# Kernel tuning notes

Hardware: AMD Instinct MI355X
Metric: run time of the kernel (lower is better)

## Reference

```python
import jax, jax.numpy as jnp
import numpy as np

B, S, D, H, T = 64, 512, 768, 384, 22  # batch, seq, bert dim, lstm hidden, tagset+2


def setup_inputs() -> dict:
    key = jax.random.key(0)
    ks = jax.random.split(key, 14)
    hidden_states = jax.random.normal(ks[0], (B, S, D), jnp.float32)
    # strictly increasing wordpiece start offsets, -1 padded (per-sample variable length)
    nw = np.array([S // 2 - (b % 16) * 4 for b in range(B)])  # number of valid start ids
    sid = -np.ones((B, S), np.int64)
    msk = np.zeros((B, S), np.int64)
    for b in range(B):
        sid[b, : nw[b]] = 1 + 2 * np.arange(nw[b])  # max = 2*nw-1 <= S-1
        msk[b, : nw[b] + 1] = 1  # word-level mask: nw+1 words incl. CLS slot
    start_ids = jnp.asarray(sid)
    masks = jnp.asarray(msk)
    sc = 0.05
    h0 = jax.random.normal(ks[1], (2, B, H), jnp.float32)
    c0 = jax.random.normal(ks[2], (2, B, H), jnp.float32)
    W_ih_f = jax.random.normal(ks[3], (4 * H, D), jnp.float32) * sc
    W_hh_f = jax.random.normal(ks[4], (4 * H, H), jnp.float32) * sc
    b_ih_f = jax.random.normal(ks[5], (4 * H,), jnp.float32) * sc
    b_hh_f = jax.random.normal(ks[6], (4 * H,), jnp.float32) * sc
    W_ih_b = jax.random.normal(ks[7], (4 * H, D), jnp.float32) * sc
    W_hh_b = jax.random.normal(ks[8], (4 * H, H), jnp.float32) * sc
    b_ih_b = jax.random.normal(ks[9], (4 * H,), jnp.float32) * sc
    b_hh_b = jax.random.normal(ks[10], (4 * H,), jnp.float32) * sc
    W_lin = jax.random.normal(ks[11], (T, 2 * H), jnp.float32) * sc
    b_lin = jax.random.normal(ks[12], (T,), jnp.float32) * sc
    return {"hidden_states": hidden_states, "h0": h0, "c0": c0,
            "W_ih_f": W_ih_f, "W_hh_f": W_hh_f, "b_ih_f": b_ih_f, "b_hh_f": b_hh_f,
            "W_ih_b": W_ih_b, "W_hh_b": W_hh_b, "b_ih_b": b_ih_b, "b_hh_b": b_hh_b,
            "W_lin": W_lin, "b_lin": b_lin, "start_ids": start_ids, "masks": masks}


def _lstm_dir(x, h0, c0, Wih, Whh, bih, bhh, reverse):
    # x: [B,S,D]; torch gate order i,f,g,o
    xg = jnp.einsum('bsd,gd->bsg', x, Wih) + bih + bhh  # [B,S,4H]
    xs = jnp.swapaxes(xg, 0, 1)  # [S,B,4H]
    if reverse:
        xs = xs[::-1]

    def step(carry, xt):
        h, c = carry
        g = xt + h @ Whh.T
        i, f, gg, o = jnp.split(g, 4, axis=-1)
        c = jax.nn.sigmoid(f) * c + jax.nn.sigmoid(i) * jnp.tanh(gg)
        h = jax.nn.sigmoid(o) * jnp.tanh(c)
        return (h, c), h

    _, hs = jax.lax.scan(step, (h0, c0), xs)
    if reverse:
        hs = hs[::-1]
    return jnp.swapaxes(hs, 0, 1)  # [B,S,H]


def _align(hidden_states, start_ids, masks):
    # word t embedding: t==0 -> token 0 (CLS); 1<=t<n -> token start_ids[t]-1
    # (last wordpiece of word t); t==n -> token start_ids[n-1]; else zero-pad.
    Bb, Ss, _ = hidden_states.shape
    t = jnp.arange(Ss)[None, :]
    valid = start_ids >= 0
    n = valid.sum(-1)  # [B] number of valid start ids
    last_sid = jnp.take_along_axis(start_ids, (n - 1)[:, None], axis=1)  # [B,1]
    idx = jnp.where(t == 0, 0,
          jnp.where(t < n[:, None], start_ids - 1,
          jnp.where(t == n[:, None], last_sid, 0)))
    idx = jnp.clip(idx, 0, Ss - 1)
    gathered = jnp.take_along_axis(hidden_states, idx[:, :, None], axis=1)
    sent_len = masks.sum(-1)  # word-level lengths (second loop in torch code)
    keep = (t < sent_len[:, None])[:, :, None]
    return jnp.where(keep, gathered, 0.0)


def reference(hidden_states, h0, c0, W_ih_f, W_hh_f, b_ih_f, b_hh_f,
              W_ih_b, W_hh_b, b_ih_b, b_hh_b, W_lin, b_lin, start_ids, masks):
    embeds = _align(hidden_states, start_ids, masks)  # q=1,k=0 => wordpiece-only
    hf = _lstm_dir(embeds, h0[0], c0[0], W_ih_f, W_hh_f, b_ih_f, b_hh_f, False)
    hb = _lstm_dir(embeds, h0[1], c0[1], W_ih_b, W_hh_b, b_ih_b, b_hh_b, True)
    lstm_out = jnp.concatenate([hf, hb], axis=-1)  # [B,S,2H]
    # dropout1 is identity in eval mode
    feats = lstm_out @ W_lin.T + b_lin  # [B,S,T]
    return feats
```

## Files before the change

### kernel.cpp

```cpp
#include <hip/hip_runtime.h>

typedef unsigned short u16;
typedef unsigned int u32;
typedef unsigned long long u64;

typedef short bf16x8 __attribute__((ext_vector_type(8)));
typedef float f32x4 __attribute__((ext_vector_type(4)));
typedef u32 u32x4 __attribute__((ext_vector_type(4)));

#define NB 64
#define NS 512
#define ND 768
#define NH 384
#define NT_OUT 22
#define S2 272
#define NG 1536
#define MGEMM (NB*S2)
#define MAGIC 0x5A5AA5A5u
#define MAX_RETRY 1000000
#define NQC 6

__device__ __forceinline__ u16 f2b(float f) {
    u32 u = __float_as_uint(f);
    u32 r = (u + 0x7fffu + ((u >> 16) & 1u)) >> 16;
    return (u16)r;
}
__device__ __forceinline__ float b2f(u16 s) { return __uint_as_float(((u32)s) << 16); }

__device__ __forceinline__ float sigm(float x) {
    return __builtin_amdgcn_rcpf(1.f + __expf(-x));
}
__device__ __forceinline__ float tanh_(float x) {
    return 1.f - 2.f * __builtin_amdgcn_rcpf(1.f + __expf(2.f * x));
}

__device__ __forceinline__ void gl_lds16(const void* g, void* l) {
    __builtin_amdgcn_global_load_lds(
        (const __attribute__((address_space(1))) unsigned int*)g,
        (__attribute__((address_space(3))) unsigned int*)l, 16, 0, 0);
}

__device__ __forceinline__ u32 ld_sc0(const int* p) {
    u32 v;
    asm volatile("global_load_dword %0, %1, off sc0 nt\n\t"
                 "s_waitcnt vmcnt(0)"
                 : "=&v"(v) : "v"(p) : "memory");
    return v;
}
__device__ __forceinline__ void st_sc0(int* p, u32 v) {
    asm volatile("global_store_dword %0, %1, off sc0" :: "v"(p), "v"(v) : "memory");
}

__device__ __forceinline__ void ld4_fast_nw(const u32* p,
        u32x4& A, u32x4& B, u32x4& C, u32x4& D) {
    asm volatile(
        "global_load_dwordx4 %0, %4, off sc0 nt\n\t"
        "global_load_dwordx4 %1, %4, off offset:16 sc0 nt\n\t"
        "global_load_dwordx4 %2, %4, off offset:128 sc0 nt\n\t"
        "global_load_dwordx4 %3, %4, off offset:144 sc0 nt"
        : "=&v"(A), "=&v"(B), "=&v"(C), "=&v"(D)
        : "v"(p) : "memory");
}
__device__ __forceinline__ void ld4_fast_wt(const u32* p,
        u32x4& A, u32x4& B, u32x4& C, u32x4& D) {
    asm volatile(
        "global_load_dwordx4 %0, %4, off sc0 nt\n\t"
        "global_load_dwordx4 %1, %4, off offset:16 sc0 nt\n\t"
        "global_load_dwordx4 %2, %4, off offset:128 sc0 nt\n\t"
        "global_load_dwordx4 %3, %4, off offset:144 sc0 nt\n\t"
        "s_waitcnt vmcnt(0)"
        : "=&v"(A), "=&v"(B), "=&v"(C), "=&v"(D)
        : "v"(p) : "memory");
}
__device__ __forceinline__ void ld4_slow(const u32* p,
        u32x4& A, u32x4& B, u32x4& C, u32x4& D) {
    #pragma unroll
    for (int e = 0; e < 4; e++) {
        A[e] = __hip_atomic_load(p + e,      __ATOMIC_RELAXED, __HIP_MEMORY_SCOPE_AGENT);
        B[e] = __hip_atomic_load(p + 4 + e,  __ATOMIC_RELAXED, __HIP_MEMORY_SCOPE_AGENT);
        C[e] = __hip_atomic_load(p + 32 + e, __ATOMIC_RELAXED, __HIP_MEMORY_SCOPE_AGENT);
        D[e] = __hip_atomic_load(p + 36 + e, __ATOMIC_RELAXED, __HIP_MEMORY_SCOPE_AGENT);
    }
}
__device__ __forceinline__ void ld4_nw(bool fast, const u32* p,
        u32x4& A, u32x4& B, u32x4& C, u32x4& D) {
    if (fast) ld4_fast_nw(p, A, B, C, D);
    else      ld4_slow(p, A, B, C, D);
}
__device__ __forceinline__ void ld4_wt(bool fast, const u32* p,
        u32x4& A, u32x4& B, u32x4& C, u32x4& D) {
    if (fast) ld4_fast_wt(p, A, B, C, D);
    else      ld4_slow(p, A, B, C, D);
}
__device__ __forceinline__ void st4(bool fast, u32* p, u32x4 v) {
    if (fast)
        asm volatile("global_store_dwordx4 %0, %1, off sc0" :: "v"(p), "v"(v) : "memory");
    else {
        #pragma unroll
        for (int e = 0; e < 4; e++)
            __hip_atomic_store(p + e, v[e], __ATOMIC_RELAXED, __HIP_MEMORY_SCOPE_AGENT);
    }
}
#define WAIT_VM(N) do { __builtin_amdgcn_sched_barrier(0); \
    asm volatile("s_waitcnt vmcnt(" #N ")" ::: "memory"); \
    __builtin_amdgcn_sched_barrier(0); } while (0)
__device__ __forceinline__ void ldsbar() {
    asm volatile("s_waitcnt lgkmcnt(0)" ::: "memory");
    __builtin_amdgcn_s_barrier();
    __builtin_amdgcn_sched_barrier(0);
}

__device__ __forceinline__ u32 sum4(const u32x4& a, const u32x4& b,
                                    const u32x4& c, const u32x4& d) {
    u32 s = (a[0] & 0xffffu) + (a[1] & 0xffffu) + (a[2] & 0xffffu) + (a[3] & 0xffffu);
    s += (b[0] & 0xffffu) + (b[1] & 0xffffu) + (b[2] & 0xffffu) + (b[3] & 0xffffu);
    s += (c[0] & 0xffffu) + (c[1] & 0xffffu) + (c[2] & 0xffffu) + (c[3] & 0xffffu);
    s += (d[0] & 0xffffu) + (d[1] & 0xffffu) + (d[2] & 0xffffu) + (d[3] & 0xffffu);
    return s;
}
__device__ __forceinline__ bf16x8 packf(const u32x4& lo, const u32x4& hi) {
    union { u32 q[4]; bf16x8 v; } U;
    U.q[0] = __builtin_amdgcn_perm(lo[1], lo[0], 0x07060302u);
    U.q[1] = __builtin_amdgcn_perm(lo[3], lo[2], 0x07060302u);
    U.q[2] = __builtin_amdgcn_perm(hi[1], hi[0], 0x07060302u);
    U.q[3] = __builtin_amdgcn_perm(hi[3], hi[2], 0x07060302u);
    return U.v;
}

__global__ void k_prep(const float* __restrict__ hidden, const int* __restrict__ start_ids,
                       const int* __restrict__ masks, u16* __restrict__ embeds) {
    int b = blockIdx.x >> 2;
    int quarter = blockIdx.x & 3;
    int tid = threadIdx.x;
    __shared__ int red[256];
    int cn = 0, cm = 0;
    for (int s = tid; s < NS; s += 256) {
        cn += (start_ids[b * NS + s] >= 0) ? 1 : 0;
        cm += (masks[b * NS + s] != 0) ? 1 : 0;
    }
    red[tid] = cn + (cm << 16);
    __syncthreads();
    #pragma unroll
    for (int off = 128; off > 0; off >>= 1) {
        if (tid < off) red[tid] += red[tid + off];
        __syncthreads();
    }
    int n = red[0] & 0xffff;
    int slen = red[0] >> 16;
    n = min(max(n, 1), NS);
    int last = start_ids[b * NS + n - 1];
    for (int t = quarter * 68; t < quarter * 68 + 68; ++t) {
        int idx;
        if (t == 0) idx = 0;
        else if (t < n) idx = start_ids[b * NS + t] - 1;
        else if (t == n) idx = last;
        else idx = 0;
        idx = min(max(idx, 0), NS - 1);
        bool keep = t < slen;
        const float* src = hidden + ((size_t)b * NS + idx) * ND;
        u16* dst = embeds + ((size_t)b * S2 + t) * ND;
        if (tid < 192) {
            float4 v = keep ? *(const float4*)(src + tid * 4) : make_float4(0.f, 0.f, 0.f, 0.f);
            union { u16 u[4]; uint2 q; } pk;
            pk.u[0] = f2b(v.x); pk.u[1] = f2b(v.y); pk.u[2] = f2b(v.z); pk.u[3] = f2b(v.w);
            *(uint2*)(dst + tid * 4) = pk.q;
        }
    }
}

__global__ void k_weights(const float* __restrict__ wf, const float* __restrict__ wb,
                          const float* __restrict__ bihf, const float* __restrict__ bhhf,
                          const float* __restrict__ bihb, const float* __restrict__ bhhb,
                          const float* __restrict__ h0,
                          u16* __restrict__ wihcat, float* __restrict__ biascat,
                          u16* __restrict__ h0buf) {
    int i0 = blockIdx.x * blockDim.x + threadIdx.x;
    int NTH = gridDim.x * blockDim.x;
    for (size_t i = i0; i < (size_t)2 * NG * ND; i += NTH) {
        size_t nrow = i / ND, k = i - nrow * ND;
        float v = (nrow < NG) ? wf[nrow * ND + k] : wb[(nrow - NG) * ND + k];
        wihcat[i] = f2b(v);
    }
    for (int i = i0; i < 2 * NG; i += NTH)
        biascat[i] = (i < NG) ? bihf[i] + bhhf[i] : bihb[i - NG] + bhhb[i - NG];
    for (int i = i0; i < 2 * NB * NH; i += NTH) h0buf[i] = f2b(h0[i]);
}

__global__ void k_packwhh(const float* __restrict__ whhf, const float* __restrict__ whhb,
                          u16* __restrict__ pack) {
    int ft = blockIdx.x * 256 + threadIdx.x;
    if (ft >= 2 * NQC * 4 * 4 * 12 * 64) return;
    int lane = ft & 63;
    int grp = ft >> 6;
    int ks = grp % 12; grp /= 12;
    int nt = grp & 3;  grp >>= 2;
    int w  = grp & 3;  grp >>= 2;
    int qc = grp % NQC;
    int d  = grp / NQC;
    const float* W = d ? whhb : whhf;
    int col = w * NH + qc * 64 + nt * 16 + (lane & 15);
    int k0 = ks * 32 + (lane >> 4) * 8;
    u16* dst = pack + (size_t)ft * 8;
    #pragma unroll
    for (int e = 0; e < 8; e++) dst[e] = f2b(W[(size_t)col * NH + k0 + e]);
}

__launch_bounds__(256, 2)
__global__ void k_gemm(const u16* __restrict__ A, const u16* __restrict__ Bw,
                       const float* __restrict__ biascat, u16* __restrict__ xg) {
    __shared__ u16 As[128 * 32];
    __shared__ u16 Bs[128 * 32];
    int tid = threadIdx.x;
    int lane = tid & 63, wid = tid >> 6;
    int l15 = lane & 15, q4 = lane >> 4;
    int bn = blockIdx.x;
    int bm = blockIdx.y;
    int wm = (wid >> 1) * 64, wn = (wid & 1) * 64;
    f32x4 acc[4][4] = {};
    for (int k0 = 0; k0 < ND; k0 += 32) {
        #pragma unroll
        for (int j = 0; j < 2; j++) {
            int fl = tid + j * 256;
            int row = fl >> 2, cb = fl & 3;
            const u16* ga = A + (size_t)(bm * 128 + row) * ND + k0 + cb * 8;
            gl_lds16(ga, &As[(size_t)(wid * 64 + j * 256) * 8]);
            const u16* gb = Bw + (size_t)(bn * 128 + row) * ND + k0 + cb * 8;
            gl_lds16(gb, &Bs[(size_t)(wid * 64 + j * 256) * 8]);
        }
        __syncthreads();
        bf16x8 af[4], bf[4];
        #pragma unroll
        for (int mt = 0; mt < 4; mt++)
            af[mt] = *(const bf16x8*)&As[(wm + mt * 16 + l15) * 32 + q4 * 8];
        #pragma unroll
        for (int nt = 0; nt < 4; nt++)
            bf[nt] = *(const bf16x8*)&Bs[(wn + nt * 16 + l15) * 32 + q4 * 8];
        #pragma unroll
        for (int mt = 0; mt < 4; mt++)
            #pragma unroll
            for (int nt = 0; nt < 4; nt++)
                acc[mt][nt] = __builtin_amdgcn_mfma_f32_16x16x32_bf16(af[mt], bf[nt], acc[mt][nt], 0, 0, 0);
        __syncthreads();
    }
    #pragma unroll
    for (int nt = 0; nt < 4; nt++) {
        int gn = bn * 128 + wn + nt * 16 + l15;
        int d = gn >= NG ? 1 : 0;
        int col = gn - d * NG;
        float bias = biascat[gn];
        #pragma unroll
        for (int mt = 0; mt < 4; mt++) {
            #pragma unroll
            for (int r = 0; r < 4; r++) {
                int m = bm * 128 + wm + mt * 16 + q4 * 4 + r;
                int b = m / S2, t = m - b * S2;
                float v = acc[mt][nt][r] + bias;
                xg[((size_t)(d * NB + b) * S2 + t) * NG + col] = f2b(v);
            }
        }
    }
}

__launch_bounds__(256, 1)
__global__ void k_recur(const u16* __restrict__ whhpack, const u16* __restrict__ xg,
                        const float* __restrict__ biascat, const u16* __restrict__ h0buf,
                        const float* __restrict__ c0, u16* __restrict__ hout,
                        int* __restrict__ flags, u32* __restrict__ xch) {
    const int blk = blockIdx.x;
    const int qc = blk >> 3;
    const int cl = blk & 7;
    const int d = cl >> 2;
    const int g = cl & 3;
    const int tid = threadIdx.x, lane = tid & 63, w = tid >> 6;
    const int q4 = lane >> 4, l15 = lane & 15;

    __shared__ float preact[4 * 16 * 68];
    __shared__ u16 hlds[16 * 72];
    __shared__ int s_fast;

    bf16x8 bfr[4][12];
    #pragma unroll
    for (int nt = 0; nt < 4; nt++)
        #pragma unroll
        for (int j = 0; j < 12; j++) {
            int ksg = 2 * ((qc + (j >> 1)) % NQC) + (j & 1);
            bfr[nt][j] = *(const bf16x8*)(whhpack +
                ((size_t)((((d * NQC + qc) * 4 + w) * 4 + nt) * 12 + ksg) * 64 + lane) * 8);
        }

    const int bb = tid >> 4;
    const int jo = (tid & 15) * 4;
    float cre[4];
    {
        const float* cp = c0 + (size_t)(d * NB + g * 16 + bb) * NH + qc * 64 + jo;
        #pragma unroll
        for (int e = 0; e < 4; e++) cre[e] = cp[e];
    }
    float biasreg[4];
    #pragma unroll
    for (int nt = 0; nt < 4; nt++)
        biasreg[nt] = biascat[d * NG + w * NH + qc * 64 + nt * 16 + l15];

    if (tid == 0) {
        int* pzb = flags + cl * 128;
        int* pmb = flags + 2048 + cl * 128;
        st_sc0(pzb + qc * 16, MAGIC);
        u32 seen = 1u << qc;
        for (int spin = 0; spin < 768 && seen != 0x3Fu; ++spin) {
            #pragma unroll
            for (int r = 0; r < NQC; ++r)
                if (!((seen >> r) & 1u) && ld_sc0(pzb + r * 16) == MAGIC) seen |= 1u << r;
            __builtin_amdgcn_s_sleep(2);
        }
        __hip_atomic_store(pmb + qc * 16, (int)(0x100u | seen),
                           __ATOMIC_RELAXED, __HIP_MEMORY_SCOPE_AGENT);
        u32 m = 0x3Fu;
        int spin2 = 0;
        #pragma unroll
        for (int r = 0; r < NQC; ++r) {
            u32 v;
            do {
                v = (u32)__hip_atomic_load(pmb + r * 16, __ATOMIC_RELAXED,
                                           __HIP_MEMORY_SCOPE_AGENT);
            } while (!(v & 0x100u) && ++spin2 < MAX_RETRY);
            m &= v;
        }
        s_fast = ((m & 0x3Fu) == 0x3Fu && spin2 < MAX_RETRY) ? 1 : 0;
    }
    __syncthreads();
    const bool fast = (s_fast != 0);

    const u16* xgd = xg + (size_t)d * NB * S2 * NG;

    float ci[4][4];
    auto preload = [&](int it2) {
        int s2 = d ? (NS - 1 - it2) : it2;
        if (s2 < S2) {
            const u16* xrow = xgd + ((size_t)(g * 16) * S2 + s2) * NG + w * NH + qc * 64 + l15;
            #pragma unroll
            for (int nt = 0; nt < 4; nt++)
                #pragma unroll
                for (int r = 0; r < 4; r++)
                    ci[nt][r] = b2f(xrow[(size_t)(q4 * 4 + r) * S2 * NG + nt * 16]);
        } else {
            #pragma unroll
            for (int nt = 0; nt < 4; nt++)
                #pragma unroll
                for (int r = 0; r < 4; r++) ci[nt][r] = biasreg[nt];
        }
    };
    preload(0);

    #pragma unroll 1
    for (int it = 0; it < NS; ++it) {
        int s = d ? (NS - 1 - it) : it;
        f32x4 acc[4];

        if (it == 0) {
            bf16x8 af0[12];
            const u16* hp = h0buf + (size_t)(d * NB + g * 16) * NH;
            #pragma unroll
            for (int j = 0; j < 12; j++) {
                int ksg = 2 * ((qc + (j >> 1)) % NQC) + (j & 1);
                af0[j] = *(const bf16x8*)(hp + (size_t)l15 * NH + ksg * 32 + q4 * 8);
            }
            #pragma unroll
            for (int nt = 0; nt < 4; nt++) {
                acc[nt][0] = ci[nt][0]; acc[nt][1] = ci[nt][1];
                acc[nt][2] = ci[nt][2]; acc[nt][3] = ci[nt][3];
            }
            preload(1);
            #pragma unroll
            for (int j = 0; j < 12; j++)
                #pragma unroll
                for (int nt = 0; nt < 4; nt++)
                    acc[nt] = __builtin_amdgcn_mfma_f32_16x16x32_bf16(af0[j], bfr[nt][j], acc[nt], 0, 0, 0);
        } else {
            const u32 T = (u32)it;
            const u32 want = T * 16u;
            u32* xb = xch + (size_t)((T & 3u) * 8 + cl) * (NQC * 1024)
                          + (u32)(l15 * 64 + q4 * 8);
            u32* p1 = xb + ((qc + 1) % NQC) * 1024;
            u32* p2 = xb + ((qc + 2) % NQC) * 1024;
            u32* p3 = xb + ((qc + 3) % NQC) * 1024;
            u32* p4 = xb + ((qc + 4) % NQC) * 1024;
            u32* p5 = xb + ((qc + 5) % NQC) * 1024;
            u32x4 r10, r11, r12, r13, r20, r21, r22, r23, r30, r31, r32, r33;
            u32x4 r40, r41, r42, r43, r50, r51, r52, r53;
            ld4_nw(fast, p1, r10, r11, r12, r13);
            ld4_nw(fast, p2, r20, r21, r22, r23);
            ld4_nw(fast, p3, r30, r31, r32, r33);
            ld4_nw(fast, p4, r40, r41, r42, r43);
            ld4_nw(fast, p5, r50, r51, r52, r53);
            bf16x8 afo0 = *(const bf16x8*)&hlds[l15 * 72 + q4 * 8];
            bf16x8 afo1 = *(const bf16x8*)&hlds[l15 * 72 + 32 + q4 * 8];
            #pragma unroll
            for (int nt = 0; nt < 4; nt++) {
                acc[nt][0] = ci[nt][0]; acc[nt][1] = ci[nt][1];
                acc[nt][2] = ci[nt][2]; acc[nt][3] = ci[nt][3];
            }
            #pragma unroll
            for (int nt = 0; nt < 4; nt++)
                acc[nt] = __builtin_amdgcn_mfma_f32_16x16x32_bf16(afo0, bfr[nt][0], acc[nt], 0, 0, 0);
            #pragma unroll
            for (int nt = 0; nt < 4; nt++)
                acc[nt] = __builtin_amdgcn_mfma_f32_16x16x32_bf16(afo1, bfr[nt][1], acc[nt], 0, 0, 0);
            int tries;
            WAIT_VM(16);
            tries = 0;
            while (!__all(sum4(r10, r11, r12, r13) == want) && ++tries < MAX_RETRY)
                ld4_wt(fast, p1, r10, r11, r12, r13);
            {
                bf16x8 lo = packf(r10, r11), hi = packf(r12, r13);
                #pragma unroll
                for (int nt = 0; nt < 4; nt++)
                    acc[nt] = __builtin_amdgcn_mfma_f32_16x16x32_bf16(lo, bfr[nt][2], acc[nt], 0, 0, 0);
                #pragma unroll
                for (int nt = 0; nt < 4; nt++)
                    acc[nt] = __builtin_amdgcn_mfma_f32_16x16x32_bf16(hi, bfr[nt][3], acc[nt], 0, 0, 0);
            }
            WAIT_VM(12);
            tries = 0;
            while (!__all(sum4(r20, r21, r22, r23) == want) && ++tries < MAX_RETRY)
                ld4_wt(fast, p2, r20, r21, r22, r23);
            {
                bf16x8 lo = packf(r20, r21), hi = packf(r22, r23);
                #pragma unroll
                for (int nt = 0; nt < 4; nt++)
                    acc[nt] = __builtin_amdgcn_mfma_f32_16x16x32_bf16(lo, bfr[nt][4], acc[nt], 0, 0, 0);
                #pragma unroll
                for (int nt = 0; nt < 4; nt++)
                    acc[nt] = __builtin_amdgcn_mfma_f32_16x16x32_bf16(hi, bfr[nt][5], acc[nt], 0, 0, 0);
            }
            WAIT_VM(8);
            tries = 0;
            while (!__all(sum4(r30, r31, r32, r33) == want) && ++tries < MAX_RETRY)
                ld4_wt(fast, p3, r30, r31, r32, r33);
            {
                bf16x8 lo = packf(r30, r31), hi = packf(r32, r33);
                #pragma unroll
                for (int nt = 0; nt < 4; nt++)
                    acc[nt] = __builtin_amdgcn_mfma_f32_16x16x32_bf16(lo, bfr[nt][6], acc[nt], 0, 0, 0);
                #pragma unroll
                for (int nt = 0; nt < 4; nt++)
                    acc[nt] = __builtin_amdgcn_mfma_f32_16x16x32_bf16(hi, bfr[nt][7], acc[nt], 0, 0, 0);
            }
            WAIT_VM(4);
            tries = 0;
            while (!__all(sum4(r40, r41, r42, r43) == want) && ++tries < MAX_RETRY)
                ld4_wt(fast, p4, r40, r41, r42, r43);
            {
                bf16x8 lo = packf(r40, r41), hi = packf(r42, r43);
                #pragma unroll
                for (int nt = 0; nt < 4; nt++)
                    acc[nt] = __builtin_amdgcn_mfma_f32_16x16x32_bf16(lo, bfr[nt][8], acc[nt], 0, 0, 0);
                #pragma unroll
                for (int nt = 0; nt < 4; nt++)
                    acc[nt] = __builtin_amdgcn_mfma_f32_16x16x32_bf16(hi, bfr[nt][9], acc[nt], 0, 0, 0);
            }
            WAIT_VM(0);
            tries = 0;
            while (!__all(sum4(r50, r51, r52, r53) == want) && ++tries < MAX_RETRY)
                ld4_wt(fast, p5, r50, r51, r52, r53);
            if (it + 1 < NS) preload(it + 1);
            {
                bf16x8 lo = packf(r50, r51), hi = packf(r52, r53);
                #pragma unroll
                for (int nt = 0; nt < 4; nt++)
                    acc[nt] = __builtin_amdgcn_mfma_f32_16x16x32_bf16(lo, bfr[nt][10], acc[nt], 0, 0, 0);
                #pragma unroll
                for (int nt = 0; nt < 4; nt++)
                    acc[nt] = __builtin_amdgcn_mfma_f32_16x16x32_bf16(hi, bfr[nt][11], acc[nt], 0, 0, 0);
            }
        }

        #pragma unroll
        for (int nt = 0; nt < 4; nt++)
            #pragma unroll
            for (int r = 0; r < 4; r++)
                preact[w * 1088 + (q4 * 4 + r) * 68 + nt * 16 + l15] = acc[nt][r];
        ldsbar();

        {
            int ib = bb * 68 + jo;
            u16* ho = hout + (((size_t)(d * NB + g * 16 + bb)) * NS + s) * NH + qc * 64 + jo;
            union { u16 u[4]; uint2 q; } pk;
            u32x4 tg;
            u32 t2 = (u32)it + 1u;
            #pragma unroll
            for (int e = 0; e < 4; e++) {
                float gi = preact[0 * 1088 + ib + e], gf = preact[1 * 1088 + ib + e];
                float gg = preact[2 * 1088 + ib + e], go = preact[3 * 1088 + ib + e];
                float c = cre[e];
                float cn = sigm(gf) * c + sigm(gi) * tanh_(gg);
                float hn = sigm(go) * tanh_(cn);
                cre[e] = cn;
                pk.u[e] = f2b(hn);
                tg[e] = ((u32)pk.u[e] << 16) | t2;
            }
            u32* xp = xch + (size_t)((t2 & 3u) * 8 + cl) * (NQC * 1024)
                          + (u32)(qc * 1024 + bb * 64 + jo);
            st4(fast, xp, tg);
            *(uint2*)ho = pk.q;
            *(uint2*)&hlds[bb * 72 + jo] = pk.q;
        }
        ldsbar();
    }
}

__global__ void k_final(const u16* __restrict__ hout, const float* __restrict__ wlin,
                        const float* __restrict__ blin, float* __restrict__ out) {
    int r = blockIdx.x * 256 + threadIdx.x;
    int b = r >> 9, t = r & 511;
    const u16* hf = hout + ((size_t)b * NS + t) * NH;
    const u16* hb = hout + ((size_t)(NB + b) * NS + t) * NH;
    float acc[NT_OUT];
    #pragma unroll
    for (int tt = 0; tt < NT_OUT; tt++) acc[tt] = blin[tt];
    #pragma unroll 1
    for (int half = 0; half < 2; half++) {
        const u16* hp = half ? hb : hf;
        #pragma unroll 1
        for (int k8 = 0; k8 < NH / 8; k8++) {
            uint4 pk = *(const uint4*)(hp + k8 * 8);
            float x[8];
            x[0] = __uint_as_float(pk.x << 16); x[1] = __uint_as_float(pk.x & 0xffff0000u);
            x[2] = __uint_as_float(pk.y << 16); x[3] = __uint_as_float(pk.y & 0xffff0000u);
            x[4] = __uint_as_float(pk.z << 16); x[5] = __uint_as_float(pk.z & 0xffff0000u);
            x[6] = __uint_as_float(pk.w << 16); x[7] = __uint_as_float(pk.w & 0xffff0000u);
            int kk = half * NH + k8 * 8;
            #pragma unroll
            for (int e = 0; e < 8; e++)
                #pragma unroll
                for (int tt = 0; tt < NT_OUT; tt++)
                    acc[tt] += x[e] * wlin[tt * (2 * NH) + kk + e];
        }
    }
    float* op = out + (size_t)r * NT_OUT;
    #pragma unroll
    for (int tt = 0; tt < NT_OUT; tt++) op[tt] = acc[tt];
}

extern "C" void kernel_launch(void* const* d_in, const int* in_sizes, int n_in,
                              void* d_out, int out_size, void* d_ws, size_t ws_size,
                              hipStream_t stream) {
    const float* hidden = (const float*)d_in[0];
    const float* h0     = (const float*)d_in[1];
    const float* c0     = (const float*)d_in[2];
    const float* Wihf   = (const float*)d_in[3];
    const float* Whhf   = (const float*)d_in[4];
    const float* bihf   = (const float*)d_in[5];
    const float* bhhf   = (const float*)d_in[6];
    const float* Wihb   = (const float*)d_in[7];
    const float* Whhb   = (const float*)d_in[8];
    const float* bihb   = (const float*)d_in[9];
    const float* bhhb   = (const float*)d_in[10];
    const float* Wlin   = (const float*)d_in[11];
    const float* blin   = (const float*)d_in[12];
    const int* start_ids = (const int*)d_in[13];
    const int* masks     = (const int*)d_in[14];
    float* out = (float*)d_out;

    char* ws = (char*)d_ws;
    size_t off = 0;
    auto alloc = [&](size_t bytes) { void* p = ws + off; off += (bytes + 255) & ~(size_t)255; return p; };
    u16* embeds   = (u16*)alloc((size_t)MGEMM * ND * 2);
    u16* wihcat   = (u16*)alloc((size_t)2 * NG * ND * 2);
    float* biascat = (float*)alloc((size_t)2 * NG * 4);
    u16* whhpack  = (u16*)alloc((size_t)2 * NG * NH * 2);
    u16* h0buf    = (u16*)alloc((size_t)2 * NB * NH * 2);
    u16* xg       = (u16*)alloc((size_t)2 * NB * S2 * NG * 2);
    u16* hout     = (u16*)alloc((size_t)2 * NB * NS * NH * 2);
    int* flags    = (int*)alloc((size_t)8 * NS * 4);
    u32* xch      = (u32*)alloc((size_t)4 * 8 * NQC * 1024 * 4);

    (void)hipMemsetAsync(flags, 0, (size_t)8 * NS * 4, stream);
    (void)hipMemsetAsync(xch, 0, (size_t)4 * 8 * NQC * 1024 * 4, stream);
    k_prep<<<256, 256, 0, stream>>>(hidden, start_ids, masks, embeds);
    k_weights<<<512, 256, 0, stream>>>(Wihf, Wihb, bihf, bhhf, bihb, bhhb, h0,
                                       wihcat, biascat, h0buf);
    k_packwhh<<<576, 256, 0, stream>>>(Whhf, Whhb, whhpack);
    dim3 ggrid(2 * NG / 128, MGEMM / 128);
    k_gemm<<<ggrid, 256, 0, stream>>>(embeds, wihcat, biascat, xg);
    k_recur<<<48, 256, 0, stream>>>(whhpack, xg, biascat, h0buf, c0, hout, flags, xch);
    k_final<<<128, 256, 0, stream>>>(hout, Wlin, blin, out);
}
```

Baseline: 2.770 ms.

## Remap recurrent MFMA tiles so each wave owns all four gates, dropping LDS exchange

```diff
diff --git a/kernel.cpp b/kernel.cpp
--- a/kernel.cpp
+++ b/kernel.cpp
@@ -92,23 +92,9 @@
     if (fast) ld4_fast_wt(p, A, B, C, D);
     else      ld4_slow(p, A, B, C, D);
 }
-__device__ __forceinline__ void st4(bool fast, u32* p, u32x4 v) {
-    if (fast)
-        asm volatile("global_store_dwordx4 %0, %1, off sc0" :: "v"(p), "v"(v) : "memory");
-    else {
-        #pragma unroll
-        for (int e = 0; e < 4; e++)
-            __hip_atomic_store(p + e, v[e], __ATOMIC_RELAXED, __HIP_MEMORY_SCOPE_AGENT);
-    }
-}
 #define WAIT_VM(N) do { __builtin_amdgcn_sched_barrier(0); \
     asm volatile("s_waitcnt vmcnt(" #N ")" ::: "memory"); \
     __builtin_amdgcn_sched_barrier(0); } while (0)
-__device__ __forceinline__ void ldsbar() {
-    asm volatile("s_waitcnt lgkmcnt(0)" ::: "memory");
-    __builtin_amdgcn_s_barrier();
-    __builtin_amdgcn_sched_barrier(0);
-}
 
 __device__ __forceinline__ u32 sum4(const u32x4& a, const u32x4& b,
                                     const u32x4& c, const u32x4& d) {
@@ -193,12 +179,12 @@
     int lane = ft & 63;
     int grp = ft >> 6;
     int ks = grp % 12; grp /= 12;
-    int nt = grp & 3;  grp >>= 2;
-    int w  = grp & 3;  grp >>= 2;
+    int gate = grp & 3; grp >>= 2;
+    int wj = grp & 3;  grp >>= 2;
     int qc = grp % NQC;
     int d  = grp / NQC;
     const float* W = d ? whhb : whhf;
-    int col = w * NH + qc * 64 + nt * 16 + (lane & 15);
+    int col = gate * NH + qc * 64 + wj * 16 + (lane & 15);
     int k0 = ks * 32 + (lane >> 4) * 8;
     u16* dst = pack + (size_t)ft * 8;
     #pragma unroll
@@ -274,32 +260,26 @@
     const int tid = threadIdx.x, lane = tid & 63, w = tid >> 6;
     const int q4 = lane >> 4, l15 = lane & 15;
 
-    __shared__ float preact[4 * 16 * 68];
-    __shared__ u16 hlds[16 * 72];
     __shared__ int s_fast;
 
     bf16x8 bfr[4][12];
     #pragma unroll
-    for (int nt = 0; nt < 4; nt++)
+    for (int gg = 0; gg < 4; gg++)
         #pragma unroll
         for (int j = 0; j < 12; j++) {
             int ksg = 2 * ((qc + (j >> 1)) % NQC) + (j & 1);
-            bfr[nt][j] = *(const bf16x8*)(whhpack +
-                ((size_t)((((d * NQC + qc) * 4 + w) * 4 + nt) * 12 + ksg) * 64 + lane) * 8);
-        }
-
-    const int bb = tid >> 4;
-    const int jo = (tid & 15) * 4;
+            bfr[gg][j] = *(const bf16x8*)(whhpack +
+                ((size_t)((((d * NQC + qc) * 4 + w) * 4 + gg) * 12 + ksg) * 64 + lane) * 8);
+        }
+
     float cre[4];
-    {
-        const float* cp = c0 + (size_t)(d * NB + g * 16 + bb) * NH + qc * 64 + jo;
-        #pragma unroll
-        for (int e = 0; e < 4; e++) cre[e] = cp[e];
-    }
+    #pragma unroll
+    for (int r = 0; r < 4; r++)
+        cre[r] = c0[(size_t)(d * NB + g * 16 + q4 * 4 + r) * NH + qc * 64 + w * 16 + l15];
     float biasreg[4];
     #pragma unroll
-    for (int nt = 0; nt < 4; nt++)
-        biasreg[nt] = biascat[d * NG + w * NH + qc * 64 + nt * 16 + l15];
+    for (int gg = 0; gg < 4; gg++)
+        biasreg[gg] = biascat[d * NG + gg * NH + qc * 64 + w * 16 + l15];
 
     if (tid == 0) {
         int* pzb = flags + cl * 128;
@@ -332,24 +312,27 @@
 
     const u16* xgd = xg + (size_t)d * NB * S2 * NG;
 
-    float ci[4][4];
-    auto preload = [&](int it2) {
+    u32 cr[4][4];
+    auto issue_preload = [&](int it2) -> bool {
         int s2 = d ? (NS - 1 - it2) : it2;
-        if (s2 < S2) {
-            const u16* xrow = xgd + ((size_t)(g * 16) * S2 + s2) * NG + w * NH + qc * 64 + l15;
-            #pragma unroll
-            for (int nt = 0; nt < 4; nt++)
-                #pragma unroll
-                for (int r = 0; r < 4; r++)
-                    ci[nt][r] = b2f(xrow[(size_t)(q4 * 4 + r) * S2 * NG + nt * 16]);
-        } else {
-            #pragma unroll
-            for (int nt = 0; nt < 4; nt++)
-                #pragma unroll
-                for (int r = 0; r < 4; r++) ci[nt][r] = biasreg[nt];
-        }
+        bool ok = (s2 >= 0) && (s2 < S2);
+        int s2c = min(max(s2, 0), S2 - 1);
+        const u16* rp = xgd + ((size_t)(g * 16 + q4 * 4) * S2 + s2c) * NG
+                        + qc * 64 + w * 16 + l15;
+        #pragma unroll
+        for (int r = 0; r < 4; r++) {
+            asm volatile(
+                "global_load_ushort %0, %4, off\n\t"
+                "global_load_ushort %1, %4, off offset:768\n\t"
+                "global_load_ushort %2, %4, off offset:1536\n\t"
+                "global_load_ushort %3, %4, off offset:2304"
+                : "=&v"(cr[0][r]), "=&v"(cr[1][r]), "=&v"(cr[2][r]), "=&v"(cr[3][r])
+                : "v"(rp) : "memory");
+            rp += (size_t)S2 * NG;
+        }
+        return ok;
     };
-    preload(0);
+    bool vld = issue_preload(0);
 
     #pragma unroll 1
     for (int it = 0; it < NS; ++it) {
@@ -357,154 +340,167 @@
         f32x4 acc[4];
 
         if (it == 0) {
-            bf16x8 af0[12];
+            WAIT_VM(0);
+            #pragma unroll
+            for (int gg = 0; gg < 4; gg++)
+                #pragma unroll
+                for (int r = 0; r < 4; r++)
+                    acc[gg][r] = vld ? __uint_as_float(cr[gg][r] << 16) : biasreg[gg];
+            vld = issue_preload(1);
             const u16* hp = h0buf + (size_t)(d * NB + g * 16) * NH;
             #pragma unroll
             for (int j = 0; j < 12; j++) {
                 int ksg = 2 * ((qc + (j >> 1)) % NQC) + (j & 1);
-                af0[j] = *(const bf16x8*)(hp + (size_t)l15 * NH + ksg * 32 + q4 * 8);
-            }
-            #pragma unroll
-            for (int nt = 0; nt < 4; nt++) {
-                acc[nt][0] = ci[nt][0]; acc[nt][1] = ci[nt][1];
-                acc[nt][2] = ci[nt][2]; acc[nt][3] = ci[nt][3];
-            }
-            preload(1);
-            #pragma unroll
-            for (int j = 0; j < 12; j++)
-                #pragma unroll
-                for (int nt = 0; nt < 4; nt++)
-                    acc[nt] = __builtin_amdgcn_mfma_f32_16x16x32_bf16(af0[j], bfr[nt][j], acc[nt], 0, 0, 0);
+                bf16x8 af = *(const bf16x8*)(hp + (size_t)l15 * NH + ksg * 32 + q4 * 8);
+                #pragma unroll
+                for (int gg = 0; gg < 4; gg++)
+                    acc[gg] = __builtin_amdgcn_mfma_f32_16x16x32_bf16(af, bfr[gg][j], acc[gg], 0, 0, 0);
+            }
         } else {
             const u32 T = (u32)it;
             const u32 want = T * 16u;
             u32* xb = xch + (size_t)((T & 3u) * 8 + cl) * (NQC * 1024)
                           + (u32)(l15 * 64 + q4 * 8);
+            u32* p0 = xb + qc * 1024;
             u32* p1 = xb + ((qc + 1) % NQC) * 1024;
             u32* p2 = xb + ((qc + 2) % NQC) * 1024;
             u32* p3 = xb + ((qc + 3) % NQC) * 1024;
             u32* p4 = xb + ((qc + 4) % NQC) * 1024;
             u32* p5 = xb + ((qc + 5) % NQC) * 1024;
-            u32x4 r10, r11, r12, r13, r20, r21, r22, r23, r30, r31, r32, r33;
-            u32x4 r40, r41, r42, r43, r50, r51, r52, r53;
+            u32x4 r00, r01, r02, r03, r10, r11, r12, r13, r20, r21, r22, r23;
+            u32x4 r30, r31, r32, r33, r40, r41, r42, r43, r50, r51, r52, r53;
+            ld4_nw(fast, p0, r00, r01, r02, r03);
             ld4_nw(fast, p1, r10, r11, r12, r13);
             ld4_nw(fast, p2, r20, r21, r22, r23);
             ld4_nw(fast, p3, r30, r31, r32, r33);
             ld4_nw(fast, p4, r40, r41, r42, r43);
             ld4_nw(fast, p5, r50, r51, r52, r53);
-            bf16x8 afo0 = *(const bf16x8*)&hlds[l15 * 72 + q4 * 8];
-            bf16x8 afo1 = *(const bf16x8*)&hlds[l15 * 72 + 32 + q4 * 8];
-            #pragma unroll
-            for (int nt = 0; nt < 4; nt++) {
-                acc[nt][0] = ci[nt][0]; acc[nt][1] = ci[nt][1];
-                acc[nt][2] = ci[nt][2]; acc[nt][3] = ci[nt][3];
-            }
-            #pragma unroll
-            for (int nt = 0; nt < 4; nt++)
-                acc[nt] = __builtin_amdgcn_mfma_f32_16x16x32_bf16(afo0, bfr[nt][0], acc[nt], 0, 0, 0);
-            #pragma unroll
-            for (int nt = 0; nt < 4; nt++)
-                acc[nt] = __builtin_amdgcn_mfma_f32_16x16x32_bf16(afo1, bfr[nt][1], acc[nt], 0, 0, 0);
+            WAIT_VM(32);
+            #pragma unroll
+            for (int gg = 0; gg < 4; gg++)
+                #pragma unroll
+                for (int r = 0; r < 4; r++)
+                    acc[gg][r] = vld ? __uint_as_float(cr[gg][r] << 16) : biasreg[gg];
+            vld = issue_preload(it + 1);
             int tries;
-            WAIT_VM(16);
+            WAIT_VM(36);
+            tries = 0;
+            while (!__all(sum4(r00, r01, r02, r03) == want) && ++tries < MAX_RETRY)
+                ld4_wt(fast, p0, r00, r01, r02, r03);
+            {
+                bf16x8 lo = packf(r00, r01), hi = packf(r02, r03);
+                #pragma unroll
+                for (int gg = 0; gg < 4; gg++)
+                    acc[gg] = __builtin_amdgcn_mfma_f32_16x16x32_bf16(lo, bfr[gg][0], acc[gg], 0, 0, 0);
+                #pragma unroll
+                for (int gg = 0; gg < 4; gg++)
+                    acc[gg] = __builtin_amdgcn_mfma_f32_16x16x32_bf16(hi, bfr[gg][1], acc[gg], 0, 0, 0);
+            }
+            WAIT_VM(32);
             tries = 0;
             while (!__all(sum4(r10, r11, r12, r13) == want) && ++tries < MAX_RETRY)
                 ld4_wt(fast, p1, r10, r11, r12, r13);
             {
                 bf16x8 lo = packf(r10, r11), hi = packf(r12, r13);
                 #pragma unroll
-                for (int nt = 0; nt < 4; nt++)
-                    acc[nt] = __builtin_amdgcn_mfma_f32_16x16x32_bf16(lo, bfr[nt][2], acc[nt], 0, 0, 0);
-                #pragma unroll
-                for (int nt = 0; nt < 4; nt++)
-                    acc[nt] = __builtin_amdgcn_mfma_f32_16x16x32_bf16(hi, bfr[nt][3], acc[nt], 0, 0, 0);
-            }
-            WAIT_VM(12);
+                for (int gg = 0; gg < 4; gg++)
+                    acc[gg] = __builtin_amdgcn_mfma_f32_16x16x32_bf16(lo, bfr[gg][2], acc[gg], 0, 0, 0);
+                #pragma unroll
+                for (int gg = 0; gg < 4; gg++)
+                    acc[gg] = __builtin_amdgcn_mfma_f32_16x16x32_bf16(hi, bfr[gg][3], acc[gg], 0, 0, 0);
+            }
+            WAIT_VM(28);
             tries = 0;
             while (!__all(sum4(r20, r21, r22, r23) == want) && ++tries < MAX_RETRY)
                 ld4_wt(fast, p2, r20, r21, r22, r23);
             {
                 bf16x8 lo = packf(r20, r21), hi = packf(r22, r23);
                 #pragma unroll
-                for (int nt = 0; nt < 4; nt++)
-                    acc[nt] = __builtin_amdgcn_mfma_f32_16x16x32_bf16(lo, bfr[nt][4], acc[nt], 0, 0, 0);
-                #pragma unroll
-                for (int nt = 0; nt < 4; nt++)
-                    acc[nt] = __builtin_amdgcn_mfma_f32_16x16x32_bf16(hi, bfr[nt][5], acc[nt], 0, 0, 0);
-            }
-            WAIT_VM(8);
+                for (int gg = 0; gg < 4; gg++)
+                    acc[gg] = __builtin_amdgcn_mfma_f32_16x16x32_bf16(lo, bfr[gg][4], acc[gg], 0, 0, 0);
+                #pragma unroll
+                for (int gg = 0; gg < 4; gg++)
+                    acc[gg] = __builtin_amdgcn_mfma_f32_16x16x32_bf16(hi, bfr[gg][5], acc[gg], 0, 0, 0);
+            }
+            WAIT_VM(24);
             tries = 0;
             while (!__all(sum4(r30, r31, r32, r33) == want) && ++tries < MAX_RETRY)
                 ld4_wt(fast, p3, r30, r31, r32, r33);
             {
                 bf16x8 lo = packf(r30, r31), hi = packf(r32, r33);
                 #pragma unroll
-                for (int nt = 0; nt < 4; nt++)
-                    acc[nt] = __builtin_amdgcn_mfma_f32_16x16x32_bf16(lo, bfr[nt][6], acc[nt], 0, 0, 0);
-                #pragma unroll
-                for (int nt = 0; nt < 4; nt++)
-                    acc[nt] = __builtin_amdgcn_mfma_f32_16x16x32_bf16(hi, bfr[nt][7], acc[nt], 0, 0, 0);
-            }
-            WAIT_VM(4);
+                for (int gg = 0; gg < 4; gg++)
+                    acc[gg] = __builtin_amdgcn_mfma_f32_16x16x32_bf16(lo, bfr[gg][6], acc[gg], 0, 0, 0);
+                #pragma unroll
+                for (int gg = 0; gg < 4; gg++)
+                    acc[gg] = __builtin_amdgcn_mfma_f32_16x16x32_bf16(hi, bfr[gg][7], acc[gg], 0, 0, 0);
+            }
+            WAIT_VM(20);
             tries = 0;
             while (!__all(sum4(r40, r41, r42, r43) == want) && ++tries < MAX_RETRY)
                 ld4_wt(fast, p4, r40, r41, r42, r43);
             {
                 bf16x8 lo = packf(r40, r41), hi = packf(r42, r43);
                 #pragma unroll
-                for (int nt = 0; nt < 4; nt++)
-                    acc[nt] = __builtin_amdgcn_mfma_f32_16x16x32_bf16(lo, bfr[nt][8], acc[nt], 0, 0, 0);
-                #pragma unroll
-                for (int nt = 0; nt < 4; nt++)
-                    acc[nt] = __builtin_amdgcn_mfma_f32_16x16x32_bf16(hi, bfr[nt][9], acc[nt], 0, 0, 0);
-            }
-            WAIT_VM(0);
+                for (int gg = 0; gg < 4; gg++)
+                    acc[gg] = __builtin_amdgcn_mfma_f32_16x16x32_bf16(lo, bfr[gg][8], acc[gg], 0, 0, 0);
+                #pragma unroll
+                for (int gg = 0; gg < 4; gg++)
+                    acc[gg] = __builtin_amdgcn_mfma_f32_16x16x32_bf16(hi, bfr[gg][9], acc[gg], 0, 0, 0);
+            }
+            WAIT_VM(16);
             tries = 0;
             while (!__all(sum4(r50, r51, r52, r53) == want) && ++tries < MAX_RETRY)
                 ld4_wt(fast, p5, r50, r51, r52, r53);
-            if (it + 1 < NS) preload(it + 1);
             {
                 bf16x8 lo = packf(r50, r51), hi = packf(r52, r53);
                 #pragma unroll
-                for (int nt = 0; nt < 4; nt++)
-                    acc[nt] = __builtin_amdgcn_mfma_f32_16x16x32_bf16(lo, bfr[nt][10], acc[nt], 0, 0, 0);
-                #pragma unroll
-                for (int nt = 0; nt < 4; nt++)
-                    acc[nt] = __builtin_amdgcn_mfma_f32_16x16x32_bf16(hi, bfr[nt][11], acc[nt], 0, 0, 0);
-            }
-        }
-
-        #pragma unroll
-        for (int nt = 0; nt < 4; nt++)
-            #pragma unroll
-            for (int r = 0; r < 4; r++)
-                preact[w * 1088 + (q4 * 4 + r) * 68 + nt * 16 + l15] = acc[nt][r];
-        ldsbar();
+                for (int gg = 0; gg < 4; gg++)
+                    acc[gg] = __builtin_amdgcn_mfma_f32_16x16x32_bf16(lo, bfr[gg][10], acc[gg], 0, 0, 0);
+                #pragma unroll
+                for (int gg = 0; gg < 4; gg++)
+                    acc[gg] = __builtin_amdgcn_mfma_f32_16x16x32_bf16(hi, bfr[gg][11], acc[gg], 0, 0, 0);
+            }
+        }
 
         {
-            int ib = bb * 68 + jo;
-            u16* ho = hout + (((size_t)(d * NB + g * 16 + bb)) * NS + s) * NH + qc * 64 + jo;
-            union { u16 u[4]; uint2 q; } pk;
-            u32x4 tg;
             u32 t2 = (u32)it + 1u;
-            #pragma unroll
-            for (int e = 0; e < 4; e++) {
-                float gi = preact[0 * 1088 + ib + e], gf = preact[1 * 1088 + ib + e];
-                float gg = preact[2 * 1088 + ib + e], go = preact[3 * 1088 + ib + e];
-                float c = cre[e];
-                float cn = sigm(gf) * c + sigm(gi) * tanh_(gg);
+            u32 tg0, tg1, tg2, tg3;
+            u16 hv[4];
+            #pragma unroll
+            for (int r = 0; r < 4; r++) {
+                float gi = acc[0][r], gf = acc[1][r];
+                float gz = acc[2][r], go = acc[3][r];
+                float c = cre[r];
+                float cn = sigm(gf) * c + sigm(gi) * tanh_(gz);
                 float hn = sigm(go) * tanh_(cn);
-                cre[e] = cn;
-                pk.u[e] = f2b(hn);
-                tg[e] = ((u32)pk.u[e] << 16) | t2;
-            }
+                cre[r] = cn;
+                hv[r] = f2b(hn);
+            }
+            tg0 = ((u32)hv[0] << 16) | t2; tg1 = ((u32)hv[1] << 16) | t2;
+            tg2 = ((u32)hv[2] << 16) | t2; tg3 = ((u32)hv[3] << 16) | t2;
+            size_t hob = ((size_t)(d * NB + g * 16 + q4 * 4) * NS + s) * NH
+                         + qc * 64 + w * 16 + l15;
+            hout[hob] = hv[0];
+            hout[hob + (size_t)NS * NH] = hv[1];
+            hout[hob + (size_t)2 * NS * NH] = hv[2];
+            hout[hob + (size_t)3 * NS * NH] = hv[3];
             u32* xp = xch + (size_t)((t2 & 3u) * 8 + cl) * (NQC * 1024)
-                          + (u32)(qc * 1024 + bb * 64 + jo);
-            st4(fast, xp, tg);
-            *(uint2*)ho = pk.q;
-            *(uint2*)&hlds[bb * 72 + jo] = pk.q;
-        }
-        ldsbar();
+                          + (u32)(qc * 1024 + (q4 * 4) * 64 + w * 16 + l15);
+            if (fast)
+                asm volatile(
+                    "global_store_dword %0, %1, off sc0\n\t"
+                    "global_store_dword %0, %2, off offset:256 sc0\n\t"
+                    "global_store_dword %0, %3, off offset:512 sc0\n\t"
+                    "global_store_dword %0, %4, off offset:768 sc0"
+                    :: "v"(xp), "v"(tg0), "v"(tg1), "v"(tg2), "v"(tg3) : "memory");
+            else {
+                __hip_atomic_store(xp,       tg0, __ATOMIC_RELAXED, __HIP_MEMORY_SCOPE_AGENT);
+                __hip_atomic_store(xp + 64,  tg1, __ATOMIC_RELAXED, __HIP_MEMORY_SCOPE_AGENT);
+                __hip_atomic_store(xp + 128, tg2, __ATOMIC_RELAXED, __HIP_MEMORY_SCOPE_AGENT);
+                __hip_atomic_store(xp + 192, tg3, __ATOMIC_RELAXED, __HIP_MEMORY_SCOPE_AGENT);
+            }
+        }
     }
 }
 
```

After: 3.215 ms. 16.1% more time.
